# Optimization experiments

Hardware: AMD Instinct MI355X
Metric: run time of the kernel (lower is better)

Reference implementation:

```python
import math
import jax, jax.numpy as jnp
import numpy as np

EPS = 1e-08
W_BLK = 256  # covers max window w = exp(log 255) + 1 = 256


def _l2norm(x):
    n = jnp.linalg.norm(x, axis=-1, keepdims=True)
    return x / jnp.maximum(n, EPS)


def setup_inputs() -> dict:
    key = jax.random.key(0)
    ks = jax.random.split(key, 7)
    B, T, Dm, H = 2, 4096, 1024, 16
    scale = 1.0 / math.sqrt(Dm)
    return {
        "query": jax.random.normal(ks[0], (B, T, Dm), jnp.float32),
        "key": jax.random.normal(ks[1], (B, T, Dm), jnp.float32),
        "value": jax.random.normal(ks[2], (B, T, Dm), jnp.float32),
        "Wq": jax.random.normal(ks[3], (Dm, Dm), jnp.float32) * scale,
        "Wk": jax.random.normal(ks[4], (Dm, Dm), jnp.float32) * scale,
        "Wv": jax.random.normal(ks[5], (Dm, Dm), jnp.float32) * scale,
        "Wo": jax.random.normal(ks[6], (Dm, Dm), jnp.float32) * scale,
        "s_v": jnp.linspace(0.0, math.log(255.0), H).astype(jnp.float32),
        "s_r": jnp.zeros((H,), jnp.float32),
    }


def _screening_forward(query, key, value, Wq, Wk, Wv, Wo, s_v, s_r):
    B, T, Dm = query.shape
    H = s_v.shape[0]
    D = Dm // H

    def proj(x, Wm):  # nn.Linear (no bias): x @ W^T, then split heads -> [B,H,T,D]
        return (x @ Wm.T).reshape(B, T, H, D).transpose(0, 2, 1, 3)

    q = _l2norm(proj(query, Wq))
    k = _l2norm(proj(key, Wk))
    v = _l2norm(proj(value, Wv))

    w = jnp.exp(s_v) + 1.0  # [H] window widths, <= 256
    r = jnp.exp(s_r) + 1.0  # [H] screening sharpness

    Wb = W_BLK
    nb = T // Wb
    qb = q.reshape(B, H, nb, Wb, D)
    kb = k.reshape(B, H, nb, Wb, D)
    vb = v.reshape(B, H, nb, Wb, D)
    # each query block attends to its own block + previous block (window <= Wb)
    kprev = jnp.pad(kb, ((0, 0), (0, 0), (1, 0), (0, 0), (0, 0)))[:, :, :nb]
    vprev = jnp.pad(vb, ((0, 0), (0, 0), (1, 0), (0, 0), (0, 0)))[:, :, :nb]
    kc = jnp.concatenate([kprev, kb], axis=3)  # [B,H,nb,2W,D]
    vc = jnp.concatenate([vprev, vb], axis=3)

    sim = jnp.einsum('bhnid,bhnjd->bhnij', qb, kc)  # [B,H,nb,W,2W]

    ii = jnp.arange(Wb)[:, None]
    jj = jnp.arange(2 * Wb)[None, :]
    rel = (jj - (Wb + ii)).astype(jnp.float32)  # [W,2W] relative offset j-i
    wb_ = w[:, None, None]  # [H,1,1]
    cos_m = 0.5 * (jnp.cos(jnp.pi * rel[None] / wb_) + 1.0)  # [H,W,2W]
    in_w = (rel[None] > -wb_) & (rel[None] <= 0.0)  # causal window
    softmask = cos_m * in_w.astype(sim.dtype)  # [H,W,2W]
    # block 0 has no previous block: first Wb key slots invalid there
    blk_valid = ((jnp.arange(nb)[:, None] > 0) | (jnp.arange(2 * Wb)[None, :] >= Wb))

    alpha = jax.nn.relu(1.0 - r[None, :, None, None, None] * (1.0 - sim)) ** 2
    alpha = alpha * softmask[None, :, None] * blk_valid.astype(sim.dtype)[None, None, :, None, :]

    out = jnp.einsum('bhnij,bhnjd->bhnid', alpha, vc).reshape(B, H, T, D)
    # TanhNorm: smoothly bound vector magnitude (tanh of the L2 norm)
    n = jnp.linalg.norm(out, axis=-1, keepdims=True)
    out = out * jnp.tanh(n) / (n + EPS)
    out = out.transpose(0, 2, 1, 3).reshape(B, T, Dm)
    return out @ Wo.T


def reference(query, key, value, Wq, Wk, Wv, Wo, s_v, s_r):
    return _screening_forward(query, key, value, Wq, Wk, Wv, Wo, s_v, s_r)
```

## Files before the change

kernel.cpp:

```cpp
#include <hip/hip_runtime.h>
#include <math.h>

#ifndef M_PI
#define M_PI 3.14159265358979323846
#endif

typedef short bf16x8 __attribute__((ext_vector_type(8)));
typedef _Float16 f16x8 __attribute__((ext_vector_type(8)));
typedef float f32x4 __attribute__((ext_vector_type(4)));

union FragU { uint4 u; bf16x8 f; };
union F16U { uint4 u; f16x8 f; _Float16 h[8]; };

typedef const __attribute__((address_space(1))) void GVoid;
typedef __attribute__((address_space(3))) void LVoid;

__device__ __forceinline__ unsigned rn_hi(float x) {
    unsigned u = __float_as_uint(x);
    unsigned r = u + 0x7FFFu + ((u >> 16) & 1u);
    return r & 0xFFFF0000u;
}

__global__ void mask_tab_kernel(const float* __restrict__ s_v, float* __restrict__ tab) {
    int h = blockIdx.x;
    int idx = threadIdx.x;
    float w = expf(s_v[h]) + 1.0f;
    float rel = (float)(idx - 255);
    float val = 0.0f;
    if (rel > -w) {
        val = 0.5f * (cosf((float)M_PI * rel / w) + 1.0f);
    }
    tab[h * 256 + idx] = val;
}

__global__ __launch_bounds__(256) void split_tiles(
        const float* __restrict__ in0, const float* __restrict__ in1,
        const float* __restrict__ in2, char* __restrict__ out0,
        unsigned long long ostride) {
    const float* in = (blockIdx.y == 0) ? in0 : (blockIdx.y == 1) ? in1 : in2;
    char* outp = out0 + (size_t)blockIdx.y * ostride;
    const int tile = blockIdx.x;
    const int kt = tile & 31;
    const int rb = tile >> 5;
    const int tid = threadIdx.x;
    const int row = tid >> 1;
    const int kc = (tid & 1) * 16;

    const float* src = in + ((size_t)(rb * 128 + row)) * 1024 + kt * 32 + kc;
    f32x4 x0 = *(const f32x4*)src;
    f32x4 x1 = *(const f32x4*)(src + 4);
    f32x4 x2 = *(const f32x4*)(src + 8);
    f32x4 x3 = *(const f32x4*)(src + 12);
    float xs[16] = {x0[0], x0[1], x0[2], x0[3], x1[0], x1[1], x1[2], x1[3],
                    x2[0], x2[1], x2[2], x2[3], x3[0], x3[1], x3[2], x3[3]};
    F16U h0, h1, l0, l1;
#pragma unroll
    for (int e = 0; e < 8; e++) {
        _Float16 h = (_Float16)xs[e];
        h0.h[e] = h;
        l0.h[e] = (_Float16)(xs[e] - (float)h);
        _Float16 h2 = (_Float16)xs[8 + e];
        h1.h[e] = h2;
        l1.h[e] = (_Float16)(xs[8 + e] - (float)h2);
    }
    char* tb = outp + (size_t)tile * 16384 + row * 128;
    const int swz = (row & 7) << 4;
    *(uint4*)(tb + ((kc * 2) ^ swz))           = h0.u;
    *(uint4*)(tb + ((kc * 2 + 16) ^ swz))      = h1.u;
    *(uint4*)(tb + ((64 + kc * 2) ^ swz))      = l0.u;
    *(uint4*)(tb + ((64 + kc * 2 + 16) ^ swz)) = l1.u;
}

__device__ __forceinline__ void cvt_split16(const f32x4* a, F16U& h0, F16U& h1,
                                            F16U& l0, F16U& l1) {
    float xs[16] = {a[0][0], a[0][1], a[0][2], a[0][3],
                    a[1][0], a[1][1], a[1][2], a[1][3],
                    a[2][0], a[2][1], a[2][2], a[2][3],
                    a[3][0], a[3][1], a[3][2], a[3][3]};
#pragma unroll
    for (int e = 0; e < 8; e++) {
        _Float16 h = (_Float16)xs[e];
        h0.h[e] = h;
        l0.h[e] = (_Float16)(xs[e] - (float)h);
        _Float16 h2 = (_Float16)xs[8 + e];
        h1.h[e] = h2;
        l1.h[e] = (_Float16)(xs[8 + e] - (float)h2);
    }
}

template <int PERM>
__global__ __launch_bounds__(256, 2) void gemm_a2(
        const float* __restrict__ A0, const float* __restrict__ A1,
        const float* __restrict__ A2,
        const char* __restrict__ Bsp, unsigned long long Bstride,
        float* __restrict__ C0, float* __restrict__ C1, float* __restrict__ C2) {
    __shared__ __align__(16) char Abuf[16384];
    __shared__ __align__(16) char Bbuf[32768];

    const int tid = threadIdx.x;
    const int bid = blockIdx.x;
    const int o = bid >> 9;
    const int x = bid & 511;
    const int xcd = x & 7;
    const int idx = x >> 3;
    const int rp = xcd * 8 + (idx >> 3);
    const int cp = idx & 7;
    const int brow = rp * 128;
    const int bcol = cp * 128;

    const float* A = (o == 0) ? A0 : (o == 1) ? A1 : A2;
    float* C = (o == 0) ? C0 : (o == 1) ? C1 : C2;
    const char* Bt = Bsp + (size_t)o * Bstride;

    const int lane = tid & 63;
    const int wid = tid >> 6;
    const int wr = wid >> 1;
    const int wc = wid & 1;
    const int l15 = lane & 15;
    const int g = lane >> 4;

    const int srow = tid >> 1;
    const int skc2 = (tid & 1) * 32;
    const float* aptr = A + (size_t)(brow + srow) * 1024 + (tid & 1) * 16;
    const int aswz = (srow & 7) << 4;
    char* awr = Abuf + srow * 128;

    const char* bsrc = Bt + ((size_t)cp * 32) * 16384 + wid * 4096;

    const int rswz = (l15 & 7) << 4;

    f32x4 acc[4][4];
#pragma unroll
    for (int a = 0; a < 4; a++)
#pragma unroll
        for (int b = 0; b < 4; b++) acc[a][b] = (f32x4)(0.0f);

    f32x4 areg[4];
    F16U Sh0, Sh1, Sl0, Sl1;

#define ISSUE_B(KT, WB)                                                        \
    do {                                                                       \
        const char* bs_ = bsrc + (size_t)(KT) * 16384;                         \
        _Pragma("unroll") for (int i = 0; i < 4; i++)                          \
            __builtin_amdgcn_global_load_lds(                                  \
                (GVoid*)(bs_ + i * 1024 + lane * 16),                          \
                (LVoid*)(Bbuf + (WB) * 16384 + wid * 4096 + i * 1024),         \
                16, 0, 0);                                                     \
    } while (0)

#define LOADA(KA)                                                              \
    do {                                                                       \
        _Pragma("unroll") for (int m = 0; m < 4; m++)                          \
            areg[m] = *(const f32x4*)(aptr + (KA) * 32 + m * 4);               \
    } while (0)

#define WRITEA()                                                               \
    do {                                                                       \
        *(uint4*)(awr + ((skc2) ^ aswz))      = Sh0.u;                         \
        *(uint4*)(awr + ((skc2 + 16) ^ aswz)) = Sh1.u;                         \
        *(uint4*)(awr + ((skc2 + 64) ^ aswz)) = Sl0.u;                         \
        *(uint4*)(awr + ((skc2 + 80) ^ aswz)) = Sl1.u;                         \
    } while (0)

#define COMPUTE(RB)                                                            \
    do {                                                                       \
        const char* bb_ = Bbuf + (RB) * 16384;                                 \
        f16x8 ah_[4], al_[4];                                                  \
        _Pragma("unroll") for (int fr = 0; fr < 4; fr++) {                     \
            const int ro_ = (wr * 64 + fr * 16 + l15) * 128;                   \
            ah_[fr] = *(const f16x8*)(Abuf + ro_ + ((g * 16) ^ rswz));         \
            al_[fr] = *(const f16x8*)(Abuf + ro_ + ((g * 16) ^ rswz ^ 64));    \
        }                                                                      \
        _Pragma("unroll") for (int fc = 0; fc < 4; fc++) {                     \
            const int ro_ = (wc * 64 + fc * 16 + l15) * 128;                   \
            f16x8 bh_ = *(const f16x8*)(bb_ + ro_ + ((g * 16) ^ rswz));        \
            f16x8 bl_ = *(const f16x8*)(bb_ + ro_ + ((g * 16) ^ rswz ^ 64));   \
            _Pragma("unroll") for (int fr = 0; fr < 4; fr++) {                 \
                acc[fr][fc] = __builtin_amdgcn_mfma_f32_16x16x32_f16(          \
                    ah_[fr], bh_, acc[fr][fc], 0, 0, 0);                       \
                acc[fr][fc] = __builtin_amdgcn_mfma_f32_16x16x32_f16(          \
                    ah_[fr], bl_, acc[fr][fc], 0, 0, 0);                       \
                acc[fr][fc] = __builtin_amdgcn_mfma_f32_16x16x32_f16(          \
                    al_[fr], bh_, acc[fr][fc], 0, 0, 0);                       \
            }                                                                  \
        }                                                                      \
    } while (0)

    LOADA(0);
    cvt_split16(areg, Sh0, Sh1, Sl0, Sl1);
    ISSUE_B(0, 0);
    WRITEA();
    __syncthreads();

#pragma unroll 1
    for (int kt = 0; kt < 32; kt += 2) {
        ISSUE_B(kt + 1, 1);
        LOADA(kt + 1);
        COMPUTE(0);
        cvt_split16(areg, Sh0, Sh1, Sl0, Sl1);
        __syncthreads();
        WRITEA();
        __syncthreads();
        if (kt + 2 < 32) { ISSUE_B(kt + 2, 0); LOADA(kt + 2); }
        COMPUTE(1);
        if (kt + 2 < 32) {
            cvt_split16(areg, Sh0, Sh1, Sl0, Sl1);
            __syncthreads();
            WRITEA();
            __syncthreads();
        }
    }

#undef COMPUTE
#undef WRITEA
#undef LOADA
#undef ISSUE_B

    if (PERM == 1) {
#pragma unroll
        for (int fr = 0; fr < 4; fr++) {
#pragma unroll
            for (int r = 0; r < 4; r++) {
                float p = 0.0f;
#pragma unroll
                for (int fc = 0; fc < 4; fc++)
                    p = fmaf(acc[fr][fc][r], acc[fr][fc][r], p);
                p += __shfl_xor(p, 1);
                p += __shfl_xor(p, 2);
                p += __shfl_xor(p, 4);
                p += __shfl_xor(p, 8);
                float inv = 1.0f / fmaxf(sqrtf(p), 1e-8f);
#pragma unroll
                for (int fc = 0; fc < 4; fc++) acc[fr][fc][r] *= inv;
            }
        }
    }

#pragma unroll
    for (int fr = 0; fr < 4; fr++) {
#pragma unroll
        for (int fc = 0; fc < 4; fc++) {
            f32x4 v = acc[fr][fc];
            const int i0 = brow + wr * 64 + fr * 16 + g * 4;
            const int j0 = bcol + wc * 64 + fc * 16;
            if (PERM == 0) {
#pragma unroll
                for (int r = 0; r < 4; r++)
                    C[(size_t)(i0 + r) * 1024 + j0 + l15] = v[r];
            } else {
                const int h = j0 >> 6;
                const int d = (j0 & 63) + l15;
#pragma unroll
                for (int r = 0; r < 4; r++) {
                    const int i = i0 + r;
                    const int b = i >> 12;
                    const int t2 = i & 4095;
                    C[(((size_t)(b * 16 + h) * 4096 + t2) * 64 + d)] = v[r];
                }
            }
        }
    }
}

__global__ __launch_bounds__(256, 3) void attn_kernel(
        const float* __restrict__ q, const float* __restrict__ k,
        const float* __restrict__ v, const float* __restrict__ s_v,
        const float* __restrict__ s_r, const float* __restrict__ mask_tab,
        float* __restrict__ out) {
    __shared__ unsigned short Kh[32 * 72];
    __shared__ unsigned short Kl[32 * 72];
    __shared__ unsigned short Vh[64 * 40];
    __shared__ unsigned short Vl[64 * 40];
    __shared__ unsigned int   aB[4][32 * 33];
    __shared__ float          msk[256];

    const int bx = blockIdx.x;
    const int h   = bx & 15;
    const int n   = (bx >> 4) & 15;
    const int sub = (bx >> 8) & 1;
    const int b   = bx >> 9;
    const int bh = b * 16 + h;
    const int tid = threadIdx.x;
    const int lane = tid & 63;
    const int wid = tid >> 6;
    const int l15 = lane & 15;
    const int g = lane >> 4;

    msk[tid] = mask_tab[h * 256 + tid];
    const float w = expf(s_v[h]) + 1.0f;
    const float rh = expf(s_r[h]) + 1.0f;

    const int row0 = n * 256 + sub * 128;
    const float* qbase = q + (size_t)bh * 4096 * 64;
    const float* kbase = k + (size_t)bh * 4096 * 64;
    const float* vbase = v + (size_t)bh * 4096 * 64;

    bf16x8 qh[2][2], ql[2][2];
#pragma unroll
    for (int f = 0; f < 2; f++) {
#pragma unroll
        for (int ks = 0; ks < 2; ks++) {
            const float* src = qbase + (size_t)(row0 + wid * 32 + f * 16 + l15) * 64
                               + ks * 32 + g * 8;
            f32x4 x0 = *(const f32x4*)src;
            f32x4 x1 = *(const f32x4*)(src + 4);
            float xs[8] = {x0[0], x0[1], x0[2], x0[3], x1[0], x1[1], x1[2], x1[3]};
            unsigned hb[8], lb[8];
#pragma unroll
            for (int e = 0; e < 8; e++) {
                hb[e] = rn_hi(xs[e]);
                lb[e] = rn_hi(xs[e] - __uint_as_float(hb[e]));
            }
            FragU th, tl;
            th.u = make_uint4((hb[0] >> 16) | hb[1], (hb[2] >> 16) | hb[3],
                              (hb[4] >> 16) | hb[5], (hb[6] >> 16) | hb[7]);
            tl.u = make_uint4((lb[0] >> 16) | lb[1], (lb[2] >> 16) | lb[3],
                              (lb[4] >> 16) | lb[5], (lb[6] >> 16) | lb[7]);
            qh[f][ks] = th.f;
            ql[f][ks] = tl.f;
        }
    }

    int jlo = (int)floorf(256.0f + (float)(sub * 128) - w) + 1;
    if (jlo < 0) jlo = 0;
    if (n == 0 && jlo < 256) jlo = 256;
    jlo &= ~31;
    const int jhi = 256 + sub * 128 + 127;

    const int iw0 = sub * 128 + wid * 32;

    f32x4 acc[2][4];
#pragma unroll
    for (int a = 0; a < 2; a++)
#pragma unroll
        for (int d = 0; d < 4; d++) acc[a][d] = (f32x4)(0.0f);

    const int kj = tid >> 3;
    const int kd = (tid & 7) * 8;
    const int vj = tid & 31;
    const int vd = (tid >> 5) * 8;

    f32x4 kr0, kr1, vr0, vr1;
    {
        const float* ks = kbase + (size_t)((n - 1) * 256 + jlo + kj) * 64 + kd;
        const float* vs = vbase + (size_t)((n - 1) * 256 + jlo + vj) * 64 + vd;
        kr0 = *(const f32x4*)ks;  kr1 = *(const f32x4*)(ks + 4);
        vr0 = *(const f32x4*)vs;  vr1 = *(const f32x4*)(vs + 4);
    }

    for (int jt = jlo; jt <= jhi; jt += 32) {
        __syncthreads();
        {
            float xs[8] = {kr0[0], kr0[1], kr0[2], kr0[3], kr1[0], kr1[1], kr1[2], kr1[3]};
            unsigned hb[8], lb[8];
#pragma unroll
            for (int e = 0; e < 8; e++) {
                hb[e] = rn_hi(xs[e]);
                lb[e] = rn_hi(xs[e] - __uint_as_float(hb[e]));
            }
            *(uint4*)&Kh[kj * 72 + kd] =
                make_uint4((hb[0] >> 16) | hb[1], (hb[2] >> 16) | hb[3],
                           (hb[4] >> 16) | hb[5], (hb[6] >> 16) | hb[7]);
            *(uint4*)&Kl[kj * 72 + kd] =
                make_uint4((lb[0] >> 16) | lb[1], (lb[2] >> 16) | lb[3],
                           (lb[4] >> 16) | lb[5], (lb[6] >> 16) | lb[7]);
        }
        {
            float xs[8] = {vr0[0], vr0[1], vr0[2], vr0[3], vr1[0], vr1[1], vr1[2], vr1[3]};
#pragma unroll
            for (int e = 0; e < 8; e++) {
                unsigned hbv = rn_hi(xs[e]);
                unsigned lbv = rn_hi(xs[e] - __uint_as_float(hbv));
                Vh[(vd + e) * 40 + vj] = (unsigned short)(hbv >> 16);
                Vl[(vd + e) * 40 + vj] = (unsigned short)(lbv >> 16);
            }
        }
        if (jt + 32 <= jhi) {
            const float* ks = kbase + (size_t)((n - 1) * 256 + jt + 32 + kj) * 64 + kd;
            const float* vs = vbase + (size_t)((n - 1) * 256 + jt + 32 + vj) * 64 + vd;
            kr0 = *(const f32x4*)ks;  kr1 = *(const f32x4*)(ks + 4);
            vr0 = *(const f32x4*)vs;  vr1 = *(const f32x4*)(vs + 4);
        }
        __syncthreads();

        const bool live = ((float)(jt + 31) > 256.0f + (float)iw0 - w) &&
                          (jt <= 256 + iw0 + 31);
        if (live) {
            f32x4 sim[2][2];
#pragma unroll
            for (int jf = 0; jf < 2; jf++)
#pragma unroll
                for (int f = 0; f < 2; f++) sim[jf][f] = (f32x4)(0.0f);

#pragma unroll
            for (int jf = 0; jf < 2; jf++) {
#pragma unroll
                for (int ks = 0; ks < 2; ks++) {
                    bf16x8 kah = *(const bf16x8*)&Kh[(jf * 16 + l15) * 72 + ks * 32 + g * 8];
                    bf16x8 kal = *(const bf16x8*)&Kl[(jf * 16 + l15) * 72 + ks * 32 + g * 8];
#pragma unroll
                    for (int f = 0; f < 2; f++) {
                        sim[jf][f] = __builtin_amdgcn_mfma_f32_16x16x32_bf16(
                            kah, qh[f][ks], sim[jf][f], 0, 0, 0);
                        sim[jf][f] = __builtin_amdgcn_mfma_f32_16x16x32_bf16(
                            kah, ql[f][ks], sim[jf][f], 0, 0, 0);
                        sim[jf][f] = __builtin_amdgcn_mfma_f32_16x16x32_bf16(
                            kal, qh[f][ks], sim[jf][f], 0, 0, 0);
                    }
                }
            }

#pragma unroll
            for (int jf = 0; jf < 2; jf++) {
#pragma unroll
                for (int f = 0; f < 2; f++) {
#pragma unroll
                    for (int r = 0; r < 4; r++) {
                        const int jloc = jf * 16 + g * 4 + r;
                        const int iloc = f * 16 + l15;
                        const int relv = (jt + jloc) - 256 - (sub * 128 + wid * 32 + iloc);
                        float m = (relv >= -255 && relv <= 0) ? msk[relv + 255] : 0.0f;
                        float t1 = 1.0f - rh * (1.0f - sim[jf][f][r]);
                        t1 = fmaxf(t1, 0.0f);
                        float alpha = t1 * t1 * m;
                        unsigned ahb = rn_hi(alpha);
                        unsigned alb = rn_hi(alpha - __uint_as_float(ahb));
                        aB[wid][jloc * 33 + iloc] = ahb | (alb >> 16);
                    }
                }
            }

#pragma unroll
            for (int f = 0; f < 2; f++) {
                unsigned a8[8];
#pragma unroll
                for (int e = 0; e < 8; e++)
                    a8[e] = aB[wid][(g * 8 + e) * 33 + f * 16 + l15];
                FragU th, tl;
                th.u = make_uint4((a8[0] >> 16) | (a8[1] & 0xFFFF0000u),
                                  (a8[2] >> 16) | (a8[3] & 0xFFFF0000u),
                                  (a8[4] >> 16) | (a8[5] & 0xFFFF0000u),
                                  (a8[6] >> 16) | (a8[7] & 0xFFFF0000u));
                tl.u = make_uint4((a8[0] << 16 >> 16) | (a8[1] << 16),
                                  (a8[2] << 16 >> 16) | (a8[3] << 16),
                                  (a8[4] << 16 >> 16) | (a8[5] << 16),
                                  (a8[6] << 16 >> 16) | (a8[7] << 16));
                bf16x8 aah = th.f, aal = tl.f;
#pragma unroll
                for (int df = 0; df < 4; df++) {
                    bf16x8 vbh = *(const bf16x8*)&Vh[(df * 16 + l15) * 40 + g * 8];
                    bf16x8 vbl = *(const bf16x8*)&Vl[(df * 16 + l15) * 40 + g * 8];
                    acc[f][df] = __builtin_amdgcn_mfma_f32_16x16x32_bf16(
                        aah, vbh, acc[f][df], 0, 0, 0);
                    acc[f][df] = __builtin_amdgcn_mfma_f32_16x16x32_bf16(
                        aah, vbl, acc[f][df], 0, 0, 0);
                    acc[f][df] = __builtin_amdgcn_mfma_f32_16x16x32_bf16(
                        aal, vbh, acc[f][df], 0, 0, 0);
                }
            }
        }
    }

#pragma unroll
    for (int f = 0; f < 2; f++) {
#pragma unroll
        for (int r = 0; r < 4; r++) {
            float p = 0.0f;
#pragma unroll
            for (int df = 0; df < 4; df++) p = fmaf(acc[f][df][r], acc[f][df][r], p);
            p += __shfl_xor(p, 1);
            p += __shfl_xor(p, 2);
            p += __shfl_xor(p, 4);
            p += __shfl_xor(p, 8);
            float nn = sqrtf(p);
            float sc = tanhf(nn) / (nn + 1e-8f);
            const int trow = row0 + wid * 32 + f * 16 + g * 4 + r;
            float* dst = out + ((size_t)(b * 4096 + trow)) * 1024 + h * 64;
#pragma unroll
            for (int df = 0; df < 4; df++)
                dst[df * 16 + l15] = acc[f][df][r] * sc;
        }
    }
}

extern "C" void kernel_launch(void* const* d_in, const int* in_sizes, int n_in,
                              void* d_out, int out_size, void* d_ws, size_t ws_size,
                              hipStream_t stream) {
    const float* query = (const float*)d_in[0];
    const float* key   = (const float*)d_in[1];
    const float* value = (const float*)d_in[2];
    const float* Wq    = (const float*)d_in[3];
    const float* Wk    = (const float*)d_in[4];
    const float* Wv    = (const float*)d_in[5];
    const float* Wo    = (const float*)d_in[6];
    const float* s_v   = (const float*)d_in[7];
    const float* s_r   = (const float*)d_in[8];
    float* out = (float*)d_out;

    const size_t MB = 1ull << 20;
    char* base = (char*)d_ws;
    float* qw   = (float*)(base);
    float* kw   = (float*)(base + 32 * MB);
    float* vw   = (float*)(base + 64 * MB);
    float* ao   = (float*)(base + 96 * MB);
    char*  w3sp = base + 96 * MB;
    char*  wosp = base;
    float* mask = (float*)(base + 128 * MB);

    mask_tab_kernel<<<dim3(16), dim3(256), 0, stream>>>(s_v, mask);

    split_tiles<<<dim3(256, 3), dim3(256), 0, stream>>>(Wq, Wk, Wv, w3sp, 4 * MB);

    gemm_a2<1><<<dim3(1536), dim3(256), 0, stream>>>(
        query, key, value, w3sp, 4 * MB, qw, kw, vw);

    attn_kernel<<<dim3(1024), dim3(256), 0, stream>>>(
        qw, kw, vw, s_v, s_r, mask, ao);

    split_tiles<<<dim3(256, 1), dim3(256), 0, stream>>>(Wo, Wo, Wo, wosp, 0);

    gemm_a2<0><<<dim3(512), dim3(256), 0, stream>>>(
        ao, ao, ao, wosp, 0, out, out, out);
}
```

Measured before the change: 308.4 us.

## Add double-buffered A-tile pipeline to QKV projection GEMM

Adds a new gemm_s1 kernel for the fused QKV projection. It double-buffers both the fp16 hi/lo split A tiles and the B tiles in LDS, so global loads and the split conversion of the next k-tile overlap the MFMA work on the current one. It uses a single barrier per stage instead of a synchronous load-then-compute pattern. LDS use doubles for A, to 64KB total, which may limit occupancy to two blocks per CU.

```diff
diff --git a/kernel.cpp b/kernel.cpp
--- a/kernel.cpp
+++ b/kernel.cpp
@@ -85,6 +85,184 @@
         _Float16 h2 = (_Float16)xs[8 + e];
         h1.h[e] = h2;
         l1.h[e] = (_Float16)(xs[8 + e] - (float)h2);
+    }
+}
+
+template <int PERM>
+__global__ __launch_bounds__(256, 2) void gemm_s1(
+        const float* __restrict__ A0, const float* __restrict__ A1,
+        const float* __restrict__ A2,
+        const char* __restrict__ Bsp, unsigned long long Bstride,
+        float* __restrict__ C0, float* __restrict__ C1, float* __restrict__ C2) {
+    __shared__ __align__(16) char Abuf[32768];
+    __shared__ __align__(16) char Bbuf[32768];
+
+    const int tid = threadIdx.x;
+    const int bid = blockIdx.x;
+    const int o = bid >> 9;
+    const int x = bid & 511;
+    const int xcd = x & 7;
+    const int idx = x >> 3;
+    const int rp = xcd * 8 + (idx >> 3);
+    const int cp = idx & 7;
+    const int brow = rp * 128;
+    const int bcol = cp * 128;
+
+    const float* A = (o == 0) ? A0 : (o == 1) ? A1 : A2;
+    float* C = (o == 0) ? C0 : (o == 1) ? C1 : C2;
+    const char* Bt = Bsp + (size_t)o * Bstride;
+
+    const int lane = tid & 63;
+    const int wid = tid >> 6;
+    const int wr = wid >> 1;
+    const int wc = wid & 1;
+    const int l15 = lane & 15;
+    const int g = lane >> 4;
+
+    const int srow = tid >> 1;
+    const int skc2 = (tid & 1) * 32;
+    const float* aptr = A + (size_t)(brow + srow) * 1024 + (tid & 1) * 16;
+    const int aswz = (srow & 7) << 4;
+    const int awro = srow * 128;
+
+    const char* bsrc = Bt + ((size_t)cp * 32) * 16384 + wid * 4096;
+
+    const int rswz = (l15 & 7) << 4;
+
+    f32x4 acc[4][4];
+#pragma unroll
+    for (int a = 0; a < 4; a++)
+#pragma unroll
+        for (int b = 0; b < 4; b++) acc[a][b] = (f32x4)(0.0f);
+
+    f32x4 areg[4];
+    F16U Sh0, Sh1, Sl0, Sl1;
+
+#define ISSUE_B(KT, WB)                                                        \
+    do {                                                                       \
+        const char* bs_ = bsrc + (size_t)(KT) * 16384;                         \
+        _Pragma("unroll") for (int i = 0; i < 4; i++)                          \
+            __builtin_amdgcn_global_load_lds(                                  \
+                (GVoid*)(bs_ + i * 1024 + lane * 16),                          \
+                (LVoid*)(Bbuf + (WB) * 16384 + wid * 4096 + i * 1024),         \
+                16, 0, 0);                                                     \
+    } while (0)
+
+#define LOADA(KA)                                                              \
+    do {                                                                       \
+        _Pragma("unroll") for (int m = 0; m < 4; m++)                          \
+            areg[m] = *(const f32x4*)(aptr + (KA) * 32 + m * 4);               \
+    } while (0)
+
+#define WRITEA(WB)                                                             \
+    do {                                                                       \
+        char* awr_ = Abuf + (WB) * 16384 + awro;                               \
+        *(uint4*)(awr_ + ((skc2) ^ aswz))      = Sh0.u;                        \
+        *(uint4*)(awr_ + ((skc2 + 16) ^ aswz)) = Sh1.u;                        \
+        *(uint4*)(awr_ + ((skc2 + 64) ^ aswz)) = Sl0.u;                        \
+        *(uint4*)(awr_ + ((skc2 + 80) ^ aswz)) = Sl1.u;                        \
+    } while (0)
+
+#define COMPUTE(RB)                                                            \
+    do {                                                                       \
+        const char* ab_ = Abuf + (RB) * 16384;                                 \
+        const char* bb_ = Bbuf + (RB) * 16384;                                 \
+        f16x8 ah_[4], al_[4];                                                  \
+        _Pragma("unroll") for (int fr = 0; fr < 4; fr++) {                     \
+            const int ro_ = (wr * 64 + fr * 16 + l15) * 128;                   \
+            ah_[fr] = *(const f16x8*)(ab_ + ro_ + ((g * 16) ^ rswz));          \
+            al_[fr] = *(const f16x8*)(ab_ + ro_ + ((g * 16) ^ rswz ^ 64));     \
+        }                                                                      \
+        _Pragma("unroll") for (int fc = 0; fc < 4; fc++) {                     \
+            const int ro_ = (wc * 64 + fc * 16 + l15) * 128;                   \
+            f16x8 bh_ = *(const f16x8*)(bb_ + ro_ + ((g * 16) ^ rswz));        \
+            f16x8 bl_ = *(const f16x8*)(bb_ + ro_ + ((g * 16) ^ rswz ^ 64));   \
+            _Pragma("unroll") for (int fr = 0; fr < 4; fr++) {                 \
+                acc[fr][fc] = __builtin_amdgcn_mfma_f32_16x16x32_f16(          \
+                    ah_[fr], bh_, acc[fr][fc], 0, 0, 0);                       \
+                acc[fr][fc] = __builtin_amdgcn_mfma_f32_16x16x32_f16(          \
+                    ah_[fr], bl_, acc[fr][fc], 0, 0, 0);                       \
+                acc[fr][fc] = __builtin_amdgcn_mfma_f32_16x16x32_f16(          \
+                    al_[fr], bh_, acc[fr][fc], 0, 0, 0);                       \
+            }                                                                  \
+        }                                                                      \
+    } while (0)
+
+    LOADA(0);
+    cvt_split16(areg, Sh0, Sh1, Sl0, Sl1);
+    ISSUE_B(0, 0);
+    WRITEA(0);
+    LOADA(1);
+    __syncthreads();
+
+#pragma unroll 1
+    for (int kt = 0; kt < 32; kt += 2) {
+        if (kt + 1 < 32) {
+            ISSUE_B(kt + 1, 1);
+            cvt_split16(areg, Sh0, Sh1, Sl0, Sl1);
+            WRITEA(1);
+            if (kt + 2 < 32) LOADA(kt + 2);
+        }
+        COMPUTE(0);
+        __syncthreads();
+        if (kt + 2 < 32) {
+            ISSUE_B(kt + 2, 0);
+            cvt_split16(areg, Sh0, Sh1, Sl0, Sl1);
+            WRITEA(0);
+            if (kt + 3 < 32) LOADA(kt + 3);
+        }
+        COMPUTE(1);
+        __syncthreads();
+    }
+
+#undef COMPUTE
+#undef WRITEA
+#undef LOADA
+#undef ISSUE_B
+
+    if (PERM == 1) {
+#pragma unroll
+        for (int fr = 0; fr < 4; fr++) {
+#pragma unroll
+            for (int r = 0; r < 4; r++) {
+                float p = 0.0f;
+#pragma unroll
+                for (int fc = 0; fc < 4; fc++)
+                    p = fmaf(acc[fr][fc][r], acc[fr][fc][r], p);
+                p += __shfl_xor(p, 1);
+                p += __shfl_xor(p, 2);
+                p += __shfl_xor(p, 4);
+                p += __shfl_xor(p, 8);
+                float inv = 1.0f / fmaxf(sqrtf(p), 1e-8f);
+#pragma unroll
+                for (int fc = 0; fc < 4; fc++) acc[fr][fc][r] *= inv;
+            }
+        }
+    }
+
+#pragma unroll
+    for (int fr = 0; fr < 4; fr++) {
+#pragma unroll
+        for (int fc = 0; fc < 4; fc++) {
+            f32x4 v = acc[fr][fc];
+            const int i0 = brow + wr * 64 + fr * 16 + g * 4;
+            const int j0 = bcol + wc * 64 + fc * 16;
+            if (PERM == 0) {
+#pragma unroll
+                for (int r = 0; r < 4; r++)
+                    C[(size_t)(i0 + r) * 1024 + j0 + l15] = v[r];
+            } else {
+                const int h = j0 >> 6;
+                const int d = (j0 & 63) + l15;
+#pragma unroll
+                for (int r = 0; r < 4; r++) {
+                    const int i = i0 + r;
+                    const int b = i >> 12;
+                    const int t2 = i & 4095;
+                    C[(((size_t)(b * 16 + h) * 4096 + t2) * 64 + d)] = v[r];
+                }
+            }
+        }
     }
 }
 
@@ -511,7 +689,7 @@
 
     split_tiles<<<dim3(256, 3), dim3(256), 0, stream>>>(Wq, Wk, Wv, w3sp, 4 * MB);
 
-    gemm_a2<1><<<dim3(1536), dim3(256), 0, stream>>>(
+    gemm_s1<1><<<dim3(1536), dim3(256), 0, stream>>>(
         query, key, value, w3sp, 4 * MB, qw, kw, vw);
 
     attn_kernel<<<dim3(1024), dim3(256), 0, stream>>>(
```

After: 311.0 us. About the same (+0.9%).
